# Kernel tuning notes

Measured on AMD Instinct MI355X. Metric: run time of the kernel, lower is better.

The kernel has to match this reference:

```python
import jax, jax.numpy as jnp
import numpy as np

N_NODES = 100000
N_EDGES = 1600000
D_FEAT = 32


def setup_inputs() -> dict:
    key = jax.random.key(0)
    k1, k2, k3 = jax.random.split(key, 3)
    features = jax.random.normal(k1, (N_NODES, D_FEAT), dtype=jnp.float32)
    src = jax.random.randint(k2, (N_EDGES,), 0, N_NODES, dtype=jnp.int64)
    dst = jax.random.randint(k3, (N_EDGES,), 0, N_NODES, dtype=jnp.int64)
    return {"features": features, "src": src, "dst": dst}


def reference(features, src, dst):
    # LightConv with norm='both' (default): symmetric degree normalization.
    n = features.shape[0]
    # out-degrees (number of edges leaving each node)
    deg = jnp.zeros((n,), dtype=features.dtype).at[src].add(1.0)
    # norm = deg^-0.5 with inf -> 0 for isolated nodes
    norm = jnp.where(deg > 0, jax.lax.rsqrt(jnp.maximum(deg, 1.0)), 0.0)[:, None]  # [N,1]
    # pre-scale (norm in ['left','both'])
    x = features * norm
    # message = copy_src, reduce = sum over incoming edges
    agg = jax.ops.segment_sum(x[src], dst, num_segments=n)  # [N,D]
    # post-scale (norm in ['right','both']) -- original reads srcdata['norm'],
    # which is the same per-node norm array for a homogeneous graph.
    return agg * norm
```

## Files before the change

### kernel.cpp

```cpp
#include <hip/hip_runtime.h>

#define D_FEAT 32
#define NPB 256
#define NPB_SHIFT 8
#define KMAX 512
#define BPART 512
#define TPART 256
#define SRC_BITS 17
#define SRC_MASK 0x1FFFF
#define CAPI 6144
#define CAP 2048


__global__ __launch_bounds__(TPART) void partition_atomic(const int* __restrict__ src,
                                                          const int* __restrict__ dst,
                                                          int* __restrict__ cntD_g,
                                                          int* __restrict__ cntS_g,
                                                          int* __restrict__ routed_d,
                                                          unsigned char* __restrict__ routed_b,
                                                          int n_edges, int K) {
    __shared__ int hD[KMAX];
    __shared__ int hS[KMAX];
    __shared__ int bD[KMAX];
    __shared__ int bS[KMAX];
    int b = blockIdx.x;
    int tid = threadIdx.x;
    for (int i = tid; i < K; i += TPART) { hD[i] = 0; hS[i] = 0; }
    __syncthreads();
    int chunk = (((n_edges + BPART - 1) / BPART) + 3) & ~3;
    int base = b * chunk;
    int eend = min(base + chunk, n_edges);
    int nvec = (eend > base) ? ((eend - base) >> 2) : 0;
    const int4* d4p = (const int4*)(dst + base);
    const int4* s4p = (const int4*)(src + base);
    for (int i = tid; i < nvec; i += TPART) {
        int4 d4 = d4p[i];
        int4 s4 = s4p[i];
        atomicAdd(&hD[d4.x >> NPB_SHIFT], 1);
        atomicAdd(&hD[d4.y >> NPB_SHIFT], 1);
        atomicAdd(&hD[d4.z >> NPB_SHIFT], 1);
        atomicAdd(&hD[d4.w >> NPB_SHIFT], 1);
        atomicAdd(&hS[s4.x >> NPB_SHIFT], 1);
        atomicAdd(&hS[s4.y >> NPB_SHIFT], 1);
        atomicAdd(&hS[s4.z >> NPB_SHIFT], 1);
        atomicAdd(&hS[s4.w >> NPB_SHIFT], 1);
    }
    for (int e = base + nvec * 4 + tid; e < eend; e += TPART) {
        atomicAdd(&hD[dst[e] >> NPB_SHIFT], 1);
        atomicAdd(&hS[src[e] >> NPB_SHIFT], 1);
    }
    __syncthreads();
    for (int i = tid; i < K; i += TPART) {
        int c = hD[i];
        bD[i] = (c > 0) ? atomicAdd(&cntD_g[i], c) : 0;
        int c2 = hS[i];
        bS[i] = (c2 > 0) ? atomicAdd(&cntS_g[i], c2) : 0;
    }
    __syncthreads();
    for (int i = tid; i < nvec; i += TPART) {
        int4 d4 = d4p[i];
        int4 s4 = s4p[i];
        int dv[4] = {d4.x, d4.y, d4.z, d4.w};
        int sv[4] = {s4.x, s4.y, s4.z, s4.w};
        #pragma unroll
        for (int u = 0; u < 4; u++) {
            int d = dv[u], s = sv[u];
            int kd = d >> NPB_SHIFT;
            int pos = atomicAdd(&bD[kd], 1);
            routed_d[(size_t)kd * CAPI + min(pos, CAPI - 1)] = ((d & (NPB - 1)) << SRC_BITS) | s;
            int ks = s >> NPB_SHIFT;
            int ps = atomicAdd(&bS[ks], 1);
            routed_b[(size_t)ks * CAPI + min(ps, CAPI - 1)] = (unsigned char)(s & (NPB - 1));
        }
    }
    for (int e = base + nvec * 4 + tid; e < eend; e += TPART) {
        int d = dst[e], s = src[e];
        int kd = d >> NPB_SHIFT;
        int pos = atomicAdd(&bD[kd], 1);
        routed_d[(size_t)kd * CAPI + min(pos, CAPI - 1)] = ((d & (NPB - 1)) << SRC_BITS) | s;
        int ks = s >> NPB_SHIFT;
        int ps = atomicAdd(&bS[ks], 1);
        routed_b[(size_t)ks * CAPI + min(ps, CAPI - 1)] = (unsigned char)(s & (NPB - 1));
    }
}

__global__ __launch_bounds__(256) void csn_prescale(const unsigned char* __restrict__ routed_b,
                                                    const int* __restrict__ cntS_g,
                                                    const float4* __restrict__ feat4,
                                                    float* __restrict__ norm,
                                                    float4* __restrict__ feat_s4,
                                                    int n_nodes, int K) {
    __shared__ int bins[NPB];
    __shared__ float nrm[NPB];
    int k = blockIdx.x;
    int tid = threadIdx.x;
    if (tid < NPB) bins[tid] = 0;
    __syncthreads();
    int beg = k * CAPI;
    int cnt = min(cntS_g[k], CAPI);
    for (int j = tid; j < cnt; j += 256)
        atomicAdd(&bins[routed_b[beg + j]], 1);
    __syncthreads();
    int kbase = k << NPB_SHIFT;
    if (tid < NPB) {
        int d = bins[tid];
        float nv = d > 0 ? rsqrtf((float)d) : 0.0f;
        nrm[tid] = nv;
        int node = kbase + tid;
        if (node < n_nodes) norm[node] = nv;
    }
    __syncthreads();
    int base4 = kbase * (D_FEAT / 4);
    for (int i = tid; i < NPB * (D_FEAT / 4); i += 256) {
        int node = kbase + (i >> 3);
        if (node < n_nodes) {
            float4 v = feat4[base4 + i];
            float nv = nrm[i >> 3];
            v.x *= nv; v.y *= nv; v.z *= nv; v.w *= nv;
            feat_s4[base4 + i] = v;
        }
    }
}

__global__ __launch_bounds__(1024) void fused_gather(const float* __restrict__ feat_s,
                                                     const int* __restrict__ routed_d,
                                                     const int* __restrict__ cntD_g,
                                                     const float* __restrict__ norm,
                                                     float* __restrict__ out,
                                                     int n_nodes, int K) {
    __shared__ int sbuf[CAP];
    __shared__ int ssort[CAP];
    __shared__ int bins[NPB];
    __shared__ int sc[NPB];
    __shared__ int off[NPB + 1];
    __shared__ int cur[NPB];
    int k = blockIdx.x;
    int tid = threadIdx.x;
    int g = tid >> 5;
    int lane = tid & 31;
    int kbase = k << NPB_SHIFT;

    int beg = k * CAPI;
    int total = min(cntD_g[k], CAPI);

    float acc[8];
    #pragma unroll
    for (int ii = 0; ii < 8; ii++) acc[ii] = 0.0f;

    for (int cb = 0; cb < total; cb += CAP) {
        int n = min(CAP, total - cb);
        __syncthreads();
        for (int i = tid; i < n; i += 1024) sbuf[i] = routed_d[beg + cb + i];
        if (tid < NPB) bins[tid] = 0;
        __syncthreads();
        for (int i = tid; i < n; i += 1024) atomicAdd(&bins[sbuf[i] >> SRC_BITS], 1);
        __syncthreads();
        if (tid < NPB) sc[tid] = bins[tid];
        __syncthreads();
        for (int st = 1; st < NPB; st <<= 1) {
            int v = (tid < NPB && tid >= st) ? sc[tid - st] : 0;
            __syncthreads();
            if (tid < NPB) sc[tid] += v;
            __syncthreads();
        }
        if (tid < NPB) {
            int ex = sc[tid] - bins[tid];
            off[tid] = ex;
            cur[tid] = ex;
        }
        if (tid == NPB - 1) off[NPB] = sc[NPB - 1];
        __syncthreads();
        for (int i = tid; i < n; i += 1024) {
            int p = sbuf[i];
            int pos = atomicAdd(&cur[p >> SRC_BITS], 1);
            ssort[pos] = p & SRC_MASK;
        }
        __syncthreads();
        #pragma unroll
        for (int ii = 0; ii < 8; ii++) {
            int dl = g + (ii << 5);
            int u0 = off[dl], u1 = off[dl + 1];
            float a = 0.0f;
            int u = u0;
            for (; u + 3 < u1; u += 4) {
                int s0 = ssort[u], s1 = ssort[u + 1], s2 = ssort[u + 2], s3 = ssort[u + 3];
                float f0 = feat_s[s0 * D_FEAT + lane];
                float f1 = feat_s[s1 * D_FEAT + lane];
                float f2 = feat_s[s2 * D_FEAT + lane];
                float f3 = feat_s[s3 * D_FEAT + lane];
                a += (f0 + f1) + (f2 + f3);
            }
            for (; u < u1; u++) a += feat_s[ssort[u] * D_FEAT + lane];
            acc[ii] += a;
        }
    }

    #pragma unroll
    for (int ii = 0; ii < 8; ii++) {
        int node = kbase + g + (ii << 5);
        if (node < n_nodes) out[(size_t)node * D_FEAT + lane] = acc[ii] * norm[node];
    }
}


__global__ void deg_kernel(const int* __restrict__ src, int* __restrict__ deg, int n_edges) {
    int e = blockIdx.x * blockDim.x + threadIdx.x;
    if (e < n_edges) atomicAdd(&deg[src[e]], 1);
}

__global__ void norm_kernel(const int* __restrict__ deg, float* __restrict__ norm, int n_nodes) {
    int i = blockIdx.x * blockDim.x + threadIdx.x;
    if (i < n_nodes) {
        int d = deg[i];
        norm[i] = d > 0 ? rsqrtf((float)d) : 0.0f;
    }
}

__global__ void scatter_kernel(const float* __restrict__ feat,
                               const int* __restrict__ src,
                               const int* __restrict__ dst,
                               const float* __restrict__ norm,
                               float* __restrict__ out, int n_edges) {
    int t = blockIdx.x * blockDim.x + threadIdx.x;
    int e = t >> 5;
    int d = t & 31;
    if (e < n_edges) {
        int s  = src[e];
        int dd = dst[e];
        float v = feat[s * D_FEAT + d] * norm[s];
        atomicAdd(&out[dd * D_FEAT + d], v);
    }
}

__global__ void post_scale_kernel(float4* __restrict__ out4,
                                  const float* __restrict__ norm, int n4) {
    int t = blockIdx.x * blockDim.x + threadIdx.x;
    if (t < n4) {
        float nv = norm[t >> 3];
        float4 v = out4[t];
        v.x *= nv; v.y *= nv; v.z *= nv; v.w *= nv;
        out4[t] = v;
    }
}


extern "C" void kernel_launch(void* const* d_in, const int* in_sizes, int n_in,
                              void* d_out, int out_size, void* d_ws, size_t ws_size,
                              hipStream_t stream) {
    const float* feat = (const float*)d_in[0];
    const int*   src  = (const int*)d_in[1];
    const int*   dst  = (const int*)d_in[2];
    float* out = (float*)d_out;

    const int n_nodes = in_sizes[0] / D_FEAT;
    const int n_edges = in_sizes[1];
    const int B = 256;

    const int K = (n_nodes + NPB - 1) >> NPB_SHIFT;

    auto align256 = [](size_t x) { return (x + 255) & ~(size_t)255; };
    size_t off = 0;
    size_t cnt_off    = off; off = align256(off + (size_t)2 * K * sizeof(int));
    size_t norm_off   = off; off = align256(off + (size_t)n_nodes * sizeof(float));
    size_t routd_off  = off; off = align256(off + (size_t)K * CAPI * sizeof(int));
    size_t routb_off  = off; off = align256(off + (size_t)K * CAPI * sizeof(unsigned char));
    size_t feats_off  = off; off = align256(off + (size_t)n_nodes * D_FEAT * sizeof(float));
    size_t needed = off;

    bool ok = (ws_size >= needed) && (K <= KMAX) && (n_nodes <= (1 << SRC_BITS));

    if (ok) {
        int*   cntD_g          = (int*)((char*)d_ws + cnt_off);
        int*   cntS_g          = cntD_g + K;
        float* norm            = (float*)((char*)d_ws + norm_off);
        int*   routed_d        = (int*)((char*)d_ws + routd_off);
        unsigned char* routed_b = (unsigned char*)((char*)d_ws + routb_off);
        float* feat_s          = (float*)((char*)d_ws + feats_off);

        hipMemsetAsync(cntD_g, 0, (size_t)2 * K * sizeof(int), stream);
        partition_atomic<<<BPART, TPART, 0, stream>>>(src, dst, cntD_g, cntS_g,
                                                      routed_d, routed_b, n_edges, K);
        csn_prescale<<<K, 256, 0, stream>>>(routed_b, cntS_g, (const float4*)feat, norm,
                                            (float4*)feat_s, n_nodes, K);
        fused_gather<<<K, 1024, 0, stream>>>(feat_s, routed_d, cntD_g, norm, out,
                                             n_nodes, K);
    } else {
        int*   deg  = (int*)d_ws;
        float* norm = (float*)((char*)d_ws + (((size_t)n_nodes * sizeof(int) + 255) & ~(size_t)255));

        hipMemsetAsync(deg, 0, (size_t)n_nodes * sizeof(int), stream);
        hipMemsetAsync(d_out, 0, (size_t)out_size * sizeof(float), stream);

        deg_kernel<<<(n_edges + B - 1) / B, B, 0, stream>>>(src, deg, n_edges);
        norm_kernel<<<(n_nodes + B - 1) / B, B, 0, stream>>>(deg, norm, n_nodes);

        long long total = (long long)n_edges * 32;
        int grid = (int)((total + B - 1) / B);
        scatter_kernel<<<grid, B, 0, stream>>>(feat, src, dst, norm, out, n_edges);

        int n4 = out_size / 4;
        post_scale_kernel<<<(n4 + B - 1) / B, B, 0, stream>>>((float4*)out, norm, n4);
    }
}
```

Before: 167.9 us.

## Split gather blocks into four 256-thread sub-blocks per destination bucket

The fused gather kernel now launches four 256-thread blocks per 256-node bucket instead of one 1024-thread block. Each sub-block owns 64 destination nodes and filters the bucket's routed edges to its quarter before its local counting sort. The intent is more, smaller blocks for better occupancy and scheduling across CUs with shorter barriers. In exchange, every sub-block reads and scans the full bucket edge list, so routed-edge loads and filtering work are repeated four times.

```diff
diff --git a/kernel.cpp b/kernel.cpp
--- a/kernel.cpp
+++ b/kernel.cpp
@@ -10,6 +10,7 @@
 #define SRC_MASK 0x1FFFF
 #define CAPI 6144
 #define CAP 2048
+#define SNODES 64
 
 
 __global__ __launch_bounds__(TPART) void partition_atomic(const int* __restrict__ src,
@@ -122,23 +123,24 @@
     }
 }
 
-__global__ __launch_bounds__(1024) void fused_gather(const float* __restrict__ feat_s,
-                                                     const int* __restrict__ routed_d,
-                                                     const int* __restrict__ cntD_g,
-                                                     const float* __restrict__ norm,
-                                                     float* __restrict__ out,
-                                                     int n_nodes, int K) {
+__global__ __launch_bounds__(256) void fused_gather(const float* __restrict__ feat_s,
+                                                    const int* __restrict__ routed_d,
+                                                    const int* __restrict__ cntD_g,
+                                                    const float* __restrict__ norm,
+                                                    float* __restrict__ out,
+                                                    int n_nodes, int K) {
     __shared__ int sbuf[CAP];
     __shared__ int ssort[CAP];
-    __shared__ int bins[NPB];
-    __shared__ int sc[NPB];
-    __shared__ int off[NPB + 1];
-    __shared__ int cur[NPB];
-    int k = blockIdx.x;
+    __shared__ int bins[SNODES];
+    __shared__ int sc[SNODES];
+    __shared__ int off[SNODES + 1];
+    __shared__ int cur[SNODES];
+    int k = blockIdx.x >> 2;
+    int q = blockIdx.x & 3;
     int tid = threadIdx.x;
     int g = tid >> 5;
     int lane = tid & 31;
-    int kbase = k << NPB_SHIFT;
+    int kbase = (k << NPB_SHIFT) + (q << 6);
 
     int beg = k * CAPI;
     int total = min(cntD_g[k], CAPI);
@@ -150,35 +152,41 @@
     for (int cb = 0; cb < total; cb += CAP) {
         int n = min(CAP, total - cb);
         __syncthreads();
-        for (int i = tid; i < n; i += 1024) sbuf[i] = routed_d[beg + cb + i];
-        if (tid < NPB) bins[tid] = 0;
-        __syncthreads();
-        for (int i = tid; i < n; i += 1024) atomicAdd(&bins[sbuf[i] >> SRC_BITS], 1);
-        __syncthreads();
-        if (tid < NPB) sc[tid] = bins[tid];
-        __syncthreads();
-        for (int st = 1; st < NPB; st <<= 1) {
-            int v = (tid < NPB && tid >= st) ? sc[tid - st] : 0;
+        for (int i = tid; i < n; i += 256) sbuf[i] = routed_d[beg + cb + i];
+        if (tid < SNODES) bins[tid] = 0;
+        __syncthreads();
+        for (int i = tid; i < n; i += 256) {
+            int dl = sbuf[i] >> SRC_BITS;
+            if ((dl >> 6) == q) atomicAdd(&bins[dl & 63], 1);
+        }
+        __syncthreads();
+        if (tid < SNODES) sc[tid] = bins[tid];
+        __syncthreads();
+        for (int st = 1; st < SNODES; st <<= 1) {
+            int v = (tid < SNODES && tid >= st) ? sc[tid - st] : 0;
             __syncthreads();
-            if (tid < NPB) sc[tid] += v;
+            if (tid < SNODES) sc[tid] += v;
             __syncthreads();
         }
-        if (tid < NPB) {
+        if (tid < SNODES) {
             int ex = sc[tid] - bins[tid];
             off[tid] = ex;
             cur[tid] = ex;
         }
-        if (tid == NPB - 1) off[NPB] = sc[NPB - 1];
-        __syncthreads();
-        for (int i = tid; i < n; i += 1024) {
+        if (tid == SNODES - 1) off[SNODES] = sc[SNODES - 1];
+        __syncthreads();
+        for (int i = tid; i < n; i += 256) {
             int p = sbuf[i];
-            int pos = atomicAdd(&cur[p >> SRC_BITS], 1);
-            ssort[pos] = p & SRC_MASK;
+            int dl = p >> SRC_BITS;
+            if ((dl >> 6) == q) {
+                int pos = atomicAdd(&cur[dl & 63], 1);
+                ssort[pos] = p & SRC_MASK;
+            }
         }
         __syncthreads();
         #pragma unroll
         for (int ii = 0; ii < 8; ii++) {
-            int dl = g + (ii << 5);
+            int dl = g + (ii << 3);
             int u0 = off[dl], u1 = off[dl + 1];
             float a = 0.0f;
             int u = u0;
@@ -197,7 +205,7 @@
 
     #pragma unroll
     for (int ii = 0; ii < 8; ii++) {
-        int node = kbase + g + (ii << 5);
+        int node = kbase + g + (ii << 3);
         if (node < n_nodes) out[(size_t)node * D_FEAT + lane] = acc[ii] * norm[node];
     }
 }
@@ -282,8 +290,8 @@
                                                       routed_d, routed_b, n_edges, K);
         csn_prescale<<<K, 256, 0, stream>>>(routed_b, cntS_g, (const float4*)feat, norm,
                                             (float4*)feat_s, n_nodes, K);
-        fused_gather<<<K, 1024, 0, stream>>>(feat_s, routed_d, cntD_g, norm, out,
-                                             n_nodes, K);
+        fused_gather<<<K * 4, 256, 0, stream>>>(feat_s, routed_d, cntD_g, norm, out,
+                                                n_nodes, K);
     } else {
         int*   deg  = (int*)d_ws;
         float* norm = (float*)((char*)d_ws + (((size_t)n_nodes * sizeof(int) + 255) & ~(size_t)255));
```

New measurement: 173.2 us. 1.03x slower.

## Fold source prescale into gather and use float4 quarter-warp feature loads

Applied to the files above, without the earlier changes.

Removes the prescaled feature buffer: the norm kernel now only computes degrees and norms, and the gather kernel multiplies each gathered row by the source norm on the fly. The gather is restructured so each 32-lane group handles four edges at once with float4 loads (8 lanes per row), followed by cross-lane shuffle reductions before the final store. This saves a full feature read/write pass and gives wider memory transactions, at the cost of an extra norm load per edge, idle lanes in tail iterations, and shuffle reductions.

```diff
diff --git a/kernel.cpp b/kernel.cpp
--- a/kernel.cpp
+++ b/kernel.cpp
@@ -84,49 +84,32 @@
     }
 }
 
-__global__ __launch_bounds__(256) void csn_prescale(const unsigned char* __restrict__ routed_b,
-                                                    const int* __restrict__ cntS_g,
-                                                    const float4* __restrict__ feat4,
-                                                    float* __restrict__ norm,
-                                                    float4* __restrict__ feat_s4,
-                                                    int n_nodes, int K) {
+__global__ __launch_bounds__(256) void count_norm(const unsigned char* __restrict__ routed_b,
+                                                  const int* __restrict__ cntS_g,
+                                                  float* __restrict__ norm,
+                                                  int n_nodes, int K) {
     __shared__ int bins[NPB];
-    __shared__ float nrm[NPB];
     int k = blockIdx.x;
     int tid = threadIdx.x;
-    if (tid < NPB) bins[tid] = 0;
+    bins[tid] = 0;
     __syncthreads();
     int beg = k * CAPI;
     int cnt = min(cntS_g[k], CAPI);
     for (int j = tid; j < cnt; j += 256)
         atomicAdd(&bins[routed_b[beg + j]], 1);
     __syncthreads();
-    int kbase = k << NPB_SHIFT;
-    if (tid < NPB) {
+    int node = (k << NPB_SHIFT) + tid;
+    if (node < n_nodes) {
         int d = bins[tid];
-        float nv = d > 0 ? rsqrtf((float)d) : 0.0f;
-        nrm[tid] = nv;
-        int node = kbase + tid;
-        if (node < n_nodes) norm[node] = nv;
-    }
-    __syncthreads();
-    int base4 = kbase * (D_FEAT / 4);
-    for (int i = tid; i < NPB * (D_FEAT / 4); i += 256) {
-        int node = kbase + (i >> 3);
-        if (node < n_nodes) {
-            float4 v = feat4[base4 + i];
-            float nv = nrm[i >> 3];
-            v.x *= nv; v.y *= nv; v.z *= nv; v.w *= nv;
-            feat_s4[base4 + i] = v;
-        }
-    }
-}
-
-__global__ __launch_bounds__(1024) void fused_gather(const float* __restrict__ feat_s,
+        norm[node] = d > 0 ? rsqrtf((float)d) : 0.0f;
+    }
+}
+
+__global__ __launch_bounds__(1024) void fused_gather(const float4* __restrict__ feat4,
                                                      const int* __restrict__ routed_d,
                                                      const int* __restrict__ cntD_g,
                                                      const float* __restrict__ norm,
-                                                     float* __restrict__ out,
+                                                     float4* __restrict__ out4,
                                                      int n_nodes, int K) {
     __shared__ int sbuf[CAP];
     __shared__ int ssort[CAP];
@@ -138,14 +121,16 @@
     int tid = threadIdx.x;
     int g = tid >> 5;
     int lane = tid & 31;
+    int sub = lane >> 3;
+    int il  = lane & 7;
     int kbase = k << NPB_SHIFT;
 
     int beg = k * CAPI;
     int total = min(cntD_g[k], CAPI);
 
-    float acc[8];
+    float4 acc[8];
     #pragma unroll
-    for (int ii = 0; ii < 8; ii++) acc[ii] = 0.0f;
+    for (int ii = 0; ii < 8; ii++) acc[ii] = make_float4(0.f, 0.f, 0.f, 0.f);
 
     for (int cb = 0; cb < total; cb += CAP) {
         int n = min(CAP, total - cb);
@@ -180,25 +165,45 @@
         for (int ii = 0; ii < 8; ii++) {
             int dl = g + (ii << 5);
             int u0 = off[dl], u1 = off[dl + 1];
-            float a = 0.0f;
+            float4 a = acc[ii];
             int u = u0;
-            for (; u + 3 < u1; u += 4) {
-                int s0 = ssort[u], s1 = ssort[u + 1], s2 = ssort[u + 2], s3 = ssort[u + 3];
-                float f0 = feat_s[s0 * D_FEAT + lane];
-                float f1 = feat_s[s1 * D_FEAT + lane];
-                float f2 = feat_s[s2 * D_FEAT + lane];
-                float f3 = feat_s[s3 * D_FEAT + lane];
-                a += (f0 + f1) + (f2 + f3);
+            for (; u + 8 <= u1; u += 8) {
+                int s0 = ssort[u + sub];
+                int s1 = ssort[u + 4 + sub];
+                float4 f0 = feat4[(size_t)s0 * 8 + il];
+                float4 f1 = feat4[(size_t)s1 * 8 + il];
+                float w0 = norm[s0];
+                float w1 = norm[s1];
+                a.x += f0.x * w0 + f1.x * w1;
+                a.y += f0.y * w0 + f1.y * w1;
+                a.z += f0.z * w0 + f1.z * w1;
+                a.w += f0.w * w0 + f1.w * w1;
             }
-            for (; u < u1; u++) a += feat_s[ssort[u] * D_FEAT + lane];
-            acc[ii] += a;
+            for (; u < u1; u += 4) {
+                if (u + sub < u1) {
+                    int s = ssort[u + sub];
+                    float4 f = feat4[(size_t)s * 8 + il];
+                    float w = norm[s];
+                    a.x += f.x * w; a.y += f.y * w; a.z += f.z * w; a.w += f.w * w;
+                }
+            }
+            acc[ii] = a;
         }
     }
 
     #pragma unroll
     for (int ii = 0; ii < 8; ii++) {
+        float4 a = acc[ii];
+        a.x += __shfl_xor(a.x, 8, 32);  a.y += __shfl_xor(a.y, 8, 32);
+        a.z += __shfl_xor(a.z, 8, 32);  a.w += __shfl_xor(a.w, 8, 32);
+        a.x += __shfl_xor(a.x, 16, 32); a.y += __shfl_xor(a.y, 16, 32);
+        a.z += __shfl_xor(a.z, 16, 32); a.w += __shfl_xor(a.w, 16, 32);
         int node = kbase + g + (ii << 5);
-        if (node < n_nodes) out[(size_t)node * D_FEAT + lane] = acc[ii] * norm[node];
+        if (node < n_nodes && lane < 8) {
+            float nv = norm[node];
+            a.x *= nv; a.y *= nv; a.z *= nv; a.w *= nv;
+            out4[(size_t)node * 8 + il] = a;
+        }
     }
 }
 
@@ -264,7 +269,6 @@
     size_t norm_off   = off; off = align256(off + (size_t)n_nodes * sizeof(float));
     size_t routd_off  = off; off = align256(off + (size_t)K * CAPI * sizeof(int));
     size_t routb_off  = off; off = align256(off + (size_t)K * CAPI * sizeof(unsigned char));
-    size_t feats_off  = off; off = align256(off + (size_t)n_nodes * D_FEAT * sizeof(float));
     size_t needed = off;
 
     bool ok = (ws_size >= needed) && (K <= KMAX) && (n_nodes <= (1 << SRC_BITS));
@@ -275,15 +279,13 @@
         float* norm            = (float*)((char*)d_ws + norm_off);
         int*   routed_d        = (int*)((char*)d_ws + routd_off);
         unsigned char* routed_b = (unsigned char*)((char*)d_ws + routb_off);
-        float* feat_s          = (float*)((char*)d_ws + feats_off);
 
         hipMemsetAsync(cntD_g, 0, (size_t)2 * K * sizeof(int), stream);
         partition_atomic<<<BPART, TPART, 0, stream>>>(src, dst, cntD_g, cntS_g,
                                                       routed_d, routed_b, n_edges, K);
-        csn_prescale<<<K, 256, 0, stream>>>(routed_b, cntS_g, (const float4*)feat, norm,
-                                            (float4*)feat_s, n_nodes, K);
-        fused_gather<<<K, 1024, 0, stream>>>(feat_s, routed_d, cntD_g, norm, out,
-                                             n_nodes, K);
+        count_norm<<<K, 256, 0, stream>>>(routed_b, cntS_g, norm, n_nodes, K);
+        fused_gather<<<K, 1024, 0, stream>>>((const float4*)feat, routed_d, cntD_g,
+                                             norm, (float4*)out, n_nodes, K);
     } else {
         int*   deg  = (int*)d_ws;
         float* norm = (float*)((char*)d_ws + (((size_t)n_nodes * sizeof(int) + 255) & ~(size_t)255));
```

Result: slower. 184.3 us (+9.8%).
